# Optimization experiments

Hardware: AMD Instinct MI355X
Metric: run time of the kernel (lower is better)

## Reference

```python
import jax, jax.numpy as jnp
import numpy as np

MAX_DISP = 4
KERNEL = 2 * MAX_DISP + 1  # 9


def setup_inputs() -> dict:
    key = jax.random.key(0)
    k1, k2 = jax.random.split(key)
    feature1 = jax.random.normal(k1, (8, 128, 128, 256), dtype=jnp.float32)
    feature2 = jax.random.normal(k2, (8, 128, 128, 256), dtype=jnp.float32)
    return {"feature1": feature1, "feature2": feature2}


def reference(feature1, feature2):
    # Windowed correlation (cost volume), equivalent to
    # unfold(feature2, k=9, pad=4) -> multiply by feature1 -> sum over channels -> /c.
    # We avoid materializing the (b, c, 81, h, w) unfolded tensor: for each of the
    # 81 displacements we slice the zero-padded feature2 and reduce over channels.
    b, c, h, w = feature1.shape
    d = MAX_DISP
    f2p = jnp.pad(feature2, ((0, 0), (0, 0), (d, d), (d, d)))  # zero padding = k//2
    corrs = []
    for ki in range(KERNEL):          # row-major kernel order, matches F.unfold
        for kj in range(KERNEL):
            shifted = f2p[:, :, ki:ki + h, kj:kj + w]          # (b, c, h, w)
            corrs.append(jnp.sum(feature1 * shifted, axis=1))  # (b, h, w)
    corr = jnp.stack(corrs, axis=1)   # (b, 81, h, w)
    return corr / c
```

## Files before the change

kernel.cpp:

```cpp
#include <hip/hip_runtime.h>


#define BB 8
#define CT 128
#define HH 128
#define WW 256
#define NK 81
#define CCH 2
#define NCHUNK (CT/CCH)
#define ROWS 9
#define LROW 264
#define LDSBUF (CCH*ROWS*LROW)

__global__ __launch_bounds__(576)
void corr_kernel(const float* __restrict__ f1, const float* __restrict__ f2,
                 float* __restrict__ out) {
    __shared__ __align__(16) float lds[2][CCH][ROWS][LROW];

    const int l   = threadIdx.x;
    const int wy  = threadIdx.y;
    const int blk = blockIdx.x;
    const int b   = blk & 7;
    const int i0  = blk >> 3;

    const int  R      = i0 - 4 + wy;
    const bool rvalid = (R >= 0) && (R < HH);

    if (rvalid) {
        if (l < 32) {
            const int buf = l >> 4, cc = (l >> 3) & 1, pos = l & 7;
            const int col = (pos < 4) ? pos : (256 + pos);
            lds[buf][cc][wy][col] = 0.f;
        }
    } else {
#pragma unroll
        for (int t = 0; t < 4; ++t)
            for (int col = l; col < LROW; col += 64)
                lds[t >> 1][t & 1][wy][col] = 0.f;
    }

    const size_t cstride = (size_t)HH * WW;
    float* lb0 = &lds[0][0][wy][4 + 4 * l];
    float* lb1 = &lds[0][1][wy][4 + 4 * l];

    float4 r0, r1;
    auto loadr = [&](int q) {
        if (rvalid) {
            const float* p = f2 + ((size_t)(b * CT + q * CCH) * HH + R) * WW + 4 * l;
            r0 = *(const float4*)p;
            r1 = *(const float4*)(p + cstride);
        }
    };
    auto storer = [&](int s) {
        if (rvalid) {
            *(float4*)(lb0 + s * LDSBUF) = r0;
            *(float4*)(lb1 + s * LDSBUF) = r1;
        }
    };

    const float* f1base = f1 + ((size_t)(b * CT) * HH + i0) * WW + 4 * l;
    auto loadf1 = [&](int q, float4& a0, float4& a1) {
        const float* p = f1base + (size_t)(q * CCH) * cstride;
        a0 = *(const float4*)p;
        a1 = *(const float4*)(p + cstride);
    };

    float acc[9][4];
#pragma unroll
    for (int d = 0; d < 9; ++d)
#pragma unroll
        for (int p = 0; p < 4; ++p) acc[d][p] = 0.f;

    auto compute = [&](int s, const float4& a0, const float4& a1) {
#pragma unroll
        for (int cc = 0; cc < CCH; ++cc) {
            const float* wp = &lds[s][cc][wy][4 * l];
            float4 w0 = *(const float4*)wp;
            float4 w1 = *(const float4*)(wp + 4);
            float4 w2 = *(const float4*)(wp + 8);
            const float4& a = cc ? a1 : a0;
            const float fv[4]   = {a.x, a.y, a.z, a.w};
            const float win[12] = {w0.x, w0.y, w0.z, w0.w,
                                   w1.x, w1.y, w1.z, w1.w,
                                   w2.x, w2.y, w2.z, w2.w};
#pragma unroll
            for (int d = 0; d < 9; ++d)
#pragma unroll
                for (int p = 0; p < 4; ++p)
                    acc[d][p] += fv[p] * win[p + d];
        }
    };

    float4 a0, a1, n0, n1;
    loadr(0);
    loadf1(0, a0, a1);
    storer(0);
    loadr(1);
    for (int q = 0; q < NCHUNK; ++q) {
        if (q + 1 < NCHUNK) storer((q + 1) & 1);
        if (q + 2 < NCHUNK) loadr(q + 2);
        if (q + 1 < NCHUNK) loadf1(q + 1, n0, n1);
        compute(q & 1, a0, a1);
        a0 = n0; a1 = n1;
    }

    const float s = 1.0f / 128.0f;
#pragma unroll
    for (int d = 0; d < 9; ++d) {
        const int k = wy * 9 + d;
        float* op = out + ((size_t)(b * NK + k) * HH + i0) * WW + 4 * l;
        *(float4*)op = make_float4(acc[d][0] * s, acc[d][1] * s,
                                   acc[d][2] * s, acc[d][3] * s);
    }
}

extern "C" void kernel_launch(void* const* d_in, const int* in_sizes, int n_in,
                              void* d_out, int out_size, void* d_ws, size_t ws_size,
                              hipStream_t stream) {
    const float* f1 = (const float*)d_in[0];
    const float* f2 = (const float*)d_in[1];
    float* out = (float*)d_out;
    dim3 grid(BB * HH);
    dim3 block(64, 9);
    hipLaunchKernelGGL(corr_kernel, grid, block, 0, stream, f1, f2, out);
}
```

Before: 418.0 us.

## Replace LDS row staging with DPP cross-lane halo exchange and independent waves

Each wavefront now loads its feature2 row straight into registers. It gets the left and right 4-column halos from neighbouring lanes with DPP wave shifts, using bound_ctrl zeroing for the image edges. This replaces the double-buffered shared-memory staging. The launch shape moves from 576-thread blocks to 256-thread blocks of independent waves, and waves whose shifted row falls outside the image write zeros and exit early. The aim is to remove LDS stores and loads and raise occupancy. In exchange it drops the explicit software prefetch and relies on the hardware keeping enough waves in flight to hide global latency.

```diff
diff --git a/kernel.cpp b/kernel.cpp
--- a/kernel.cpp
+++ b/kernel.cpp
@@ -1,69 +1,43 @@
 #include <hip/hip_runtime.h>
 
 
-#define BB 8
 #define CT 128
 #define HH 128
 #define WW 256
 #define NK 81
-#define CCH 2
-#define NCHUNK (CT/CCH)
-#define ROWS 9
-#define LROW 264
-#define LDSBUF (CCH*ROWS*LROW)
+#define HW ((size_t)HH * WW)
 
-__global__ __launch_bounds__(576)
+__device__ __forceinline__ float halo_left(float x) {
+    return __int_as_float(__builtin_amdgcn_update_dpp(
+        0, __float_as_int(x), 0x138, 0xF, 0xF, true));
+}
+__device__ __forceinline__ float halo_right(float x) {
+    return __int_as_float(__builtin_amdgcn_update_dpp(
+        0, __float_as_int(x), 0x130, 0xF, 0xF, true));
+}
+
+__global__ __launch_bounds__(256, 6)
 void corr_kernel(const float* __restrict__ f1, const float* __restrict__ f2,
                  float* __restrict__ out) {
-    __shared__ __align__(16) float lds[2][CCH][ROWS][LROW];
+    const int l  = threadIdx.x & 63;
+    const int gw = blockIdx.x * 4 + (threadIdx.x >> 6);
+    const int wy = gw % 9;
+    const int bi = gw / 9;
+    const int i0 = bi & (HH - 1);
+    const int b  = bi >> 7;
+    const int R  = i0 - 4 + wy;
 
-    const int l   = threadIdx.x;
-    const int wy  = threadIdx.y;
-    const int blk = blockIdx.x;
-    const int b   = blk & 7;
-    const int i0  = blk >> 3;
+    float* op = out + ((size_t)(b * NK + wy * 9) * HH + i0) * WW + 4 * l;
 
-    const int  R      = i0 - 4 + wy;
-    const bool rvalid = (R >= 0) && (R < HH);
-
-    if (rvalid) {
-        if (l < 32) {
-            const int buf = l >> 4, cc = (l >> 3) & 1, pos = l & 7;
-            const int col = (pos < 4) ? pos : (256 + pos);
-            lds[buf][cc][wy][col] = 0.f;
-        }
-    } else {
+    if ((unsigned)R >= (unsigned)HH) {
+        const float4 z = make_float4(0.f, 0.f, 0.f, 0.f);
 #pragma unroll
-        for (int t = 0; t < 4; ++t)
-            for (int col = l; col < LROW; col += 64)
-                lds[t >> 1][t & 1][wy][col] = 0.f;
+        for (int d = 0; d < 9; ++d) *(float4*)(op + (size_t)d * HW) = z;
+        return;
     }
 
-    const size_t cstride = (size_t)HH * WW;
-    float* lb0 = &lds[0][0][wy][4 + 4 * l];
-    float* lb1 = &lds[0][1][wy][4 + 4 * l];
-
-    float4 r0, r1;
-    auto loadr = [&](int q) {
-        if (rvalid) {
-            const float* p = f2 + ((size_t)(b * CT + q * CCH) * HH + R) * WW + 4 * l;
-            r0 = *(const float4*)p;
-            r1 = *(const float4*)(p + cstride);
-        }
-    };
-    auto storer = [&](int s) {
-        if (rvalid) {
-            *(float4*)(lb0 + s * LDSBUF) = r0;
-            *(float4*)(lb1 + s * LDSBUF) = r1;
-        }
-    };
-
-    const float* f1base = f1 + ((size_t)(b * CT) * HH + i0) * WW + 4 * l;
-    auto loadf1 = [&](int q, float4& a0, float4& a1) {
-        const float* p = f1base + (size_t)(q * CCH) * cstride;
-        a0 = *(const float4*)p;
-        a1 = *(const float4*)(p + cstride);
-    };
+    const float* p1 = f1 + ((size_t)b * CT * HH + i0) * WW + 4 * l;
+    const float* p2 = f2 + ((size_t)b * CT * HH + R) * WW + 4 * l;
 
     float acc[9][4];
 #pragma unroll
@@ -71,47 +45,38 @@
 #pragma unroll
         for (int p = 0; p < 4; ++p) acc[d][p] = 0.f;
 
-    auto compute = [&](int s, const float4& a0, const float4& a1) {
+    for (int q = 0; q < CT / 2; ++q) {
+        const float4 a0 = *(const float4*)p1;
+        const float4 a1 = *(const float4*)(p1 + HW);
+        const float4 b0 = *(const float4*)p2;
+        const float4 b1 = *(const float4*)(p2 + HW);
+        p1 += 2 * HW;
+        p2 += 2 * HW;
 #pragma unroll
-        for (int cc = 0; cc < CCH; ++cc) {
-            const float* wp = &lds[s][cc][wy][4 * l];
-            float4 w0 = *(const float4*)wp;
-            float4 w1 = *(const float4*)(wp + 4);
-            float4 w2 = *(const float4*)(wp + 8);
+        for (int cc = 0; cc < 2; ++cc) {
             const float4& a = cc ? a1 : a0;
-            const float fv[4]   = {a.x, a.y, a.z, a.w};
-            const float win[12] = {w0.x, w0.y, w0.z, w0.w,
-                                   w1.x, w1.y, w1.z, w1.w,
-                                   w2.x, w2.y, w2.z, w2.w};
+            const float4& r = cc ? b1 : b0;
+            float w[12];
+            w[0]  = halo_left(r.x);  w[1]  = halo_left(r.y);
+            w[2]  = halo_left(r.z);  w[3]  = halo_left(r.w);
+            w[4]  = r.x;             w[5]  = r.y;
+            w[6]  = r.z;             w[7]  = r.w;
+            w[8]  = halo_right(r.x); w[9]  = halo_right(r.y);
+            w[10] = halo_right(r.z); w[11] = halo_right(r.w);
+            const float fv[4] = {a.x, a.y, a.z, a.w};
 #pragma unroll
             for (int d = 0; d < 9; ++d)
 #pragma unroll
                 for (int p = 0; p < 4; ++p)
-                    acc[d][p] += fv[p] * win[p + d];
+                    acc[d][p] += fv[p] * w[p + d];
         }
-    };
-
-    float4 a0, a1, n0, n1;
-    loadr(0);
-    loadf1(0, a0, a1);
-    storer(0);
-    loadr(1);
-    for (int q = 0; q < NCHUNK; ++q) {
-        if (q + 1 < NCHUNK) storer((q + 1) & 1);
-        if (q + 2 < NCHUNK) loadr(q + 2);
-        if (q + 1 < NCHUNK) loadf1(q + 1, n0, n1);
-        compute(q & 1, a0, a1);
-        a0 = n0; a1 = n1;
     }
 
     const float s = 1.0f / 128.0f;
 #pragma unroll
-    for (int d = 0; d < 9; ++d) {
-        const int k = wy * 9 + d;
-        float* op = out + ((size_t)(b * NK + k) * HH + i0) * WW + 4 * l;
-        *(float4*)op = make_float4(acc[d][0] * s, acc[d][1] * s,
-                                   acc[d][2] * s, acc[d][3] * s);
-    }
+    for (int d = 0; d < 9; ++d)
+        *(float4*)(op + (size_t)d * HW) =
+            make_float4(acc[d][0] * s, acc[d][1] * s, acc[d][2] * s, acc[d][3] * s);
 }
 
 extern "C" void kernel_launch(void* const* d_in, const int* in_sizes, int n_in,
@@ -120,7 +85,7 @@
     const float* f1 = (const float*)d_in[0];
     const float* f2 = (const float*)d_in[1];
     float* out = (float*)d_out;
-    dim3 grid(BB * HH);
-    dim3 block(64, 9);
+    dim3 grid(2304);
+    dim3 block(256);
     hipLaunchKernelGGL(corr_kernel, grid, block, 0, stream, f1, f2, out);
 }
```

Result: slower. 450.6 us (+7.8%).
